# Kernel tuning notes

Measured on AMD Instinct MI355X. Metric: run time of the kernel, lower is better.

The kernel has to match this reference:

```python
import jax, jax.numpy as jnp
import numpy as np

V = 200000   # total vertices
K = 96       # neighbours per vertex (incl. self)
NSEG = 4     # number of row-split segments


def setup_inputs() -> dict:
    key = jax.random.key(0)
    k1, k2 = jax.random.split(key)
    seg_size = V // NSEG
    row_splits = (jnp.arange(NSEG + 1, dtype=jnp.int32) * seg_size)
    seg_id = jnp.repeat(jnp.arange(NSEG, dtype=jnp.int32), seg_size)
    seg_start = row_splits[seg_id]                      # (V,)
    # segment-local random neighbours, self index in column 0 (kNN convention)
    offs = jax.random.randint(k1, (V, K), 0, seg_size, dtype=jnp.int32)
    neighs = seg_start[:, None] + offs
    neighs = neighs.at[:, 0].set(jnp.arange(V, dtype=jnp.int32))
    hier = jax.random.uniform(k2, (V, 1), dtype=jnp.float32)
    return {"neighs": neighs, "hier": hier, "row_splits": row_splits}


def _cluster(neighs, hier, row_splits):
    """Greedy hierarchy-ordered neighbour clustering (NMS-like).

    Returns:
      sel     (V,1) int32: cluster-centre vertex indices, compacted to the
              front in processing order, padded with -1 (original op returns
              a dynamically sized tensor; we pad for fixed shapes).
      rs      (n_seg+1,) int32: row splits after selection.
      ggather (V,1) int32: for each vertex, the position in `sel` of its
              cluster centre (gather-back indices).
    """
    Vn, _ = neighs.shape
    n_seg = row_splits.shape[0] - 1
    seg_id = jnp.searchsorted(row_splits[1:], jnp.arange(Vn), side='right').astype(jnp.int32)
    # per-segment argsort descending on hier, with global offsets == global
    # lexsort by (segment, -hier) since vertices are segment-contiguous
    order = jnp.lexsort((-hier[:, 0], seg_id)).astype(jnp.int32)  # (V,)

    def step(assign, v):
        is_new = assign[v] < 0                 # v not yet absorbed -> new centre
        nb = neighs[v]                          # (K,) neighbour indices
        grab = is_new & (assign[nb] < 0)        # unassigned neighbours get taken
        assign = assign.at[jnp.where(is_new, v, Vn)].set(v, mode='drop')
        assign = assign.at[jnp.where(grab, nb, Vn)].set(v, mode='drop')
        return assign, is_new

    assign0 = jnp.full((Vn,), -1, jnp.int32)
    assign, is_new = jax.lax.scan(step, assign0, order)  # assign: centre vertex per vertex

    new_i = is_new.astype(jnp.int32)
    pos = jnp.cumsum(new_i) - 1                           # rank of each centre in order
    sel = jnp.full((Vn,), -1, jnp.int32).at[jnp.where(is_new, pos, Vn)].set(order, mode='drop')
    counts = jax.ops.segment_sum(new_i, seg_id[order], num_segments=n_seg)
    rs = jnp.concatenate([jnp.zeros((1,), jnp.int32), jnp.cumsum(counts).astype(jnp.int32)])
    center_rank = jnp.zeros((Vn,), jnp.int32).at[jnp.where(is_new, order, Vn)].set(pos, mode='drop')
    ggather = center_rank[assign].reshape(-1, 1)
    return sel.reshape(-1, 1), rs, ggather


def reference(neighs, hier, row_splits):
    return _cluster(neighs, hier, row_splits)
```

## Files before the change

### kernel.cpp

```cpp
#include <hip/hip_runtime.h>

#define IDX_BITS 20
#define IDX_MASK ((1u << IDX_BITS) - 1)
#define NT1 1024
#define MAX_G1 512
#define T1 49152
#define TB2 16
#define T2 4096
#define T3CAP 4096
#define GRID_ROUND_CAP 16
#define MAX_ROUNDS 8000
#define SC_CAP 1024
#define SV_CAP 4096

typedef unsigned long long u64;

__device__ __forceinline__ u64 pack_key(float h, int v) {
  return ((u64)(~__float_as_uint(h)) << IDX_BITS) | (unsigned)v;
}

__device__ __forceinline__ int ald(const int* p) {
  return __hip_atomic_load((int*)p, __ATOMIC_RELAXED, __HIP_MEMORY_SCOPE_AGENT);
}
__device__ __forceinline__ u64 ald64(const u64* p) {
  return __hip_atomic_load((u64*)p, __ATOMIC_RELAXED, __HIP_MEMORY_SCOPE_AGENT);
}
__device__ __forceinline__ void ast(int* p, int v) {
  __hip_atomic_store(p, v, __ATOMIC_RELAXED, __HIP_MEMORY_SCOPE_AGENT);
}

struct Ctx {
  const int* __restrict__ neighs;
  const float* __restrict__ hier;
  const int* __restrict__ row_splits;
  int V, K, nseg;
  u64* assign;
  int* tag;
  int* listA;
  int* listB;
  u64* centre_key;
  int* centre_v;
  int* rank_of;
  int* cnt;
  int* out_sel;
  int* out_rs;
  int* out_gg;
};

struct BlkState {
  int sc_cnt, sv_cnt, sc_base, sv_base;
  int seg_hist[8];
  int sc_list[SC_CAP];
  int sv_list[SV_CAP];
};

__device__ __forceinline__ void xbar(int* bar, int target) {
  __syncthreads();
  if (threadIdx.x == 0) {
    __builtin_amdgcn_fence(__ATOMIC_RELEASE, "agent");
    __hip_atomic_fetch_add(bar, 1, __ATOMIC_RELAXED, __HIP_MEMORY_SCOPE_AGENT);
    while (__hip_atomic_load(bar, __ATOMIC_RELAXED, __HIP_MEMORY_SCOPE_AGENT) < target)
      __builtin_amdgcn_s_sleep(2);
  }
  __syncthreads();
}

__device__ __forceinline__ void record_direct(const Ctx& c, int v, u64 pv) {
  int slot = atomicAdd(&c.cnt[4], 1);
  int seg = 0;
  for (int t = 1; t < c.nseg; ++t) seg += (v >= c.row_splits[t]);
  c.centre_v[slot] = v;
  c.centre_key[slot] = ((u64)seg << 52) | pv;
  atomicAdd(&c.cnt[8 + seg], 1);
}

__device__ __forceinline__ void phaseB(const Ctx& c, const int* rl, int an, int r,
                                       int qs, int qst, int ql) {
  if (c.K == 96) {
    for (int i = qs; i < an; i += qst) {
      int u = rl ? ald(&rl[i]) : i;
      u64 pu = pack_key(c.hier[u], u);
      if (rl && ald64(&c.assign[u]) <= pu) continue;
      const int* row = c.neighs + (size_t)u * 96;
      int w[6];
#pragma unroll
      for (int t = 0; t < 6; ++t) w[t] = row[ql + 16 * t];
#pragma unroll
      for (int t = 0; t < 6; ++t)
        if (pack_key(c.hier[w[t]], w[t]) > pu) c.tag[w[t]] = r;
    }
  } else {
    for (int i = qs; i < an; i += qst) {
      int u = rl ? ald(&rl[i]) : i;
      u64 pu = pack_key(c.hier[u], u);
      if (rl && ald64(&c.assign[u]) <= pu) continue;
      const int* row = c.neighs + (size_t)u * c.K;
      for (int j = ql; j < c.K; j += 16) {
        int w = row[j];
        if (pack_key(c.hier[w], w) > pu) c.tag[w] = r;
      }
    }
  }
}

__device__ __forceinline__ void phaseC(const Ctx& c, BlkState& bs, const int* rl,
                                       int* wl, int* survc, int an, int r,
                                       int qs, int qst, int ql) {
  for (int i = qs; i < an; i += qst) {
    int u = rl ? ald(&rl[i]) : i;
    u64 pu = pack_key(c.hier[u], u);
    if (ald64(&c.assign[u]) <= pu) continue;
    if (ald(&c.tag[u]) != r) {
      const int* row = c.neighs + (size_t)u * c.K;
      if (c.K == 96) {
#pragma unroll
        for (int t = 0; t < 6; ++t) atomicMin(&c.assign[row[ql + 16 * t]], pu);
      } else {
        for (int j = ql; j < c.K; j += 16) atomicMin(&c.assign[row[j]], pu);
      }
      if (ql == 0) {
        int s = atomicAdd(&bs.sc_cnt, 1);
        if (s < SC_CAP) bs.sc_list[s] = u; else record_direct(c, u, pu);
      }
    } else if (ql == 0) {
      u64 y = ald64(&c.assign[u]);
      if (y > pu) {
        int s = atomicAdd(&bs.sv_cnt, 1);
        if (s < SV_CAP) bs.sv_list[s] = u;
        else { int g = atomicAdd(survc, 1); wl[g] = u; }
      }
    }
  }
}

__device__ __forceinline__ void flush_block(const Ctx& c, BlkState& bs, int* wl, int* survc) {
  __syncthreads();
  int nsc = min(bs.sc_cnt, SC_CAP), nsv = min(bs.sv_cnt, SV_CAP);
  if (threadIdx.x == 0 && nsc) bs.sc_base = atomicAdd(&c.cnt[4], nsc);
  if (threadIdx.x == 0 && nsv) bs.sv_base = atomicAdd(survc, nsv);
  if (threadIdx.x < 8) bs.seg_hist[threadIdx.x] = 0;
  __syncthreads();
  for (int i = threadIdx.x; i < nsv; i += blockDim.x) wl[bs.sv_base + i] = bs.sv_list[i];
  for (int i = threadIdx.x; i < nsc; i += blockDim.x) {
    int v = bs.sc_list[i];
    int seg = 0;
    for (int t = 1; t < c.nseg; ++t) seg += (v >= c.row_splits[t]);
    c.centre_v[bs.sc_base + i] = v;
    c.centre_key[bs.sc_base + i] = ((u64)seg << 52) | pack_key(c.hier[v], v);
    atomicAdd(&bs.seg_hist[seg], 1);
  }
  __syncthreads();
  if (threadIdx.x < c.nseg) {
    int h = bs.seg_hist[threadIdx.x];
    if (h) atomicAdd(&c.cnt[8 + threadIdx.x], h);
  }
  __syncthreads();
  if (threadIdx.x == 0) { bs.sc_cnt = 0; bs.sv_cnt = 0; }
}

__global__ void __launch_bounds__(NT1) k_tier1(Ctx c) {
  __shared__ BlkState bs;
  const int tid = blockIdx.x * blockDim.x + threadIdx.x;
  const int nthr = gridDim.x * blockDim.x;
  const int ql = threadIdx.x & 15;
  const int qg = tid >> 4, nq = nthr >> 4;
  const int nb = gridDim.x;
  if (threadIdx.x == 0) { bs.sc_cnt = 0; bs.sv_cnt = 0; }
  __syncthreads();

  int aliveN = c.V, r = 0, ep = 0;
  while (true) {
    const int* rl = (r & 1) ? c.listA : c.listB;
    int* wl = (r & 1) ? c.listB : c.listA;
    if (tid == 0) ast(&c.cnt[(r + 1) & 1], 0);
    phaseB(c, r ? rl : nullptr, aliveN, r, qg, nq, ql);
    xbar(&c.cnt[16], nb * (++ep));
    phaseC(c, bs, r ? rl : nullptr, wl, &c.cnt[(r + 1) & 1], aliveN, r, qg, nq, ql);
    flush_block(c, bs, wl, &c.cnt[(r + 1) & 1]);
    xbar(&c.cnt[16], nb * (++ep));
    aliveN = ald(&c.cnt[(r + 1) & 1]);
    ++r;
    if (aliveN == 0 || aliveN <= T1 || r >= GRID_ROUND_CAP) break;
  }
  if (tid == 0) { ast(&c.cnt[5], aliveN); ast(&c.cnt[6], r); }
}

__global__ void __launch_bounds__(NT1) k_tier2(Ctx c) {
  __shared__ BlkState bs;
  const int ql = threadIdx.x & 15;
  const int NBQ = NT1 >> 4;
  if (threadIdx.x == 0) { bs.sc_cnt = 0; bs.sv_cnt = 0; }
  __syncthreads();

  int an = ald(&c.cnt[5]), tr = ald(&c.cnt[6]);
  if (an <= T2) return;

  const int qstart = blockIdx.x * NBQ + (threadIdx.x >> 4);
  const int qstride = TB2 * NBQ;
  int ep = 0;
  while (true) {
    const int* rl = (tr & 1) ? c.listA : c.listB;
    int* wl = (tr & 1) ? c.listB : c.listA;
    if (blockIdx.x == 0 && threadIdx.x == 0) ast(&c.cnt[(tr + 1) & 1], 0);
    phaseB(c, rl, an, tr, qstart, qstride, ql);
    xbar(&c.cnt[32], TB2 * (++ep));
    phaseC(c, bs, rl, wl, &c.cnt[(tr + 1) & 1], an, tr, qstart, qstride, ql);
    flush_block(c, bs, wl, &c.cnt[(tr + 1) & 1]);
    xbar(&c.cnt[32], TB2 * (++ep));
    an = ald(&c.cnt[(tr + 1) & 1]);
    ++tr;
    if (an == 0 || an <= T2 || tr >= MAX_ROUNDS) break;
  }
  if (blockIdx.x == 0 && threadIdx.x == 0) { ast(&c.cnt[5], an); ast(&c.cnt[6], tr); }
}

__global__ void __launch_bounds__(NT1) k_tier3(Ctx c) {
  __shared__ int fr[T3CAP];
  __shared__ int tg[T3CAP];
  __shared__ unsigned char dd[T3CAP];
  __shared__ int tmp[T3CAP];
  __shared__ int nnew;
  const int ql = threadIdx.x & 15;
  const int bq = threadIdx.x >> 4;
  const int NBQ = NT1 >> 4;

  int an = ald(&c.cnt[5]);
  int tr = ald(&c.cnt[6]);
  if (an <= 0 || an > T3CAP) return;
  const int* rl = (tr & 1) ? c.listA : c.listB;

  for (int i = threadIdx.x; i < an; i += NT1) {
    int v = ald(&rl[i]);
    u64 pv = pack_key(c.hier[v], v);
    fr[i] = v;
    tg[i] = -1;
    dd[i] = (ald64(&c.assign[v]) <= pv) ? 1 : 0;
    c.rank_of[v] = i;
  }
  __syncthreads();

  int r = tr;
  while (an > 0 && r < MAX_ROUNDS) {
    for (int i = bq; i < an; i += NBQ) {
      if (dd[i]) continue;
      int u = fr[i];
      u64 pu = pack_key(c.hier[u], u);
      const int* row = c.neighs + (size_t)u * c.K;
      for (int j = ql; j < c.K; j += 16) {
        int w = row[j];
        if (pack_key(c.hier[w], w) > pu) {
          int s = c.rank_of[w];
          if ((unsigned)s < (unsigned)an && fr[s] == w) tg[s] = r;
        }
      }
    }
    __syncthreads();
    for (int i = bq; i < an; i += NBQ) {
      if (dd[i]) continue;
      if (tg[i] != r) {
        int u = fr[i];
        u64 pu = pack_key(c.hier[u], u);
        const int* row = c.neighs + (size_t)u * c.K;
        for (int j = ql; j < c.K; j += 16) {
          int w = row[j];
          atomicMin(&c.assign[w], pu);
          if (pack_key(c.hier[w], w) > pu) {
            int s = c.rank_of[w];
            if ((unsigned)s < (unsigned)an && fr[s] == w) dd[s] = 1;
          }
        }
        if (ql == 0) { dd[i] = 1; record_direct(c, u, pu); }
      }
    }
    __syncthreads();
    if (threadIdx.x == 0) nnew = 0;
    __syncthreads();
    for (int i = threadIdx.x; i < an; i += NT1) {
      if (!dd[i]) { int j = atomicAdd(&nnew, 1); tmp[j] = fr[i]; }
    }
    __syncthreads();
    an = nnew;
    __syncthreads();
    for (int i = threadIdx.x; i < an; i += NT1) {
      int v = tmp[i];
      fr[i] = v; tg[i] = -1; dd[i] = 0;
      c.rank_of[v] = i;
    }
    __syncthreads();
    ++r;
  }
}

__global__ void __launch_bounds__(NT1) k_rank(Ctx c) {
  __shared__ u64 shp[NT1];
  const int nC = c.cnt[4];
  for (int base = blockIdx.x * NT1; base < nC; base += gridDim.x * NT1) {
    int idx = base + threadIdx.x;
    bool have = idx < nC;
    u64 mykey = have ? c.centre_key[idx] : 0;
    int myv = have ? c.centre_v[idx] : 0;
    int myrank = 0;
    for (int cs = 0; cs < nC; cs += NT1) {
      int j = cs + threadIdx.x;
      shp[threadIdx.x] = (j < nC) ? c.centre_key[j] : ~0ull;
      __syncthreads();
      int lim = min(NT1, nC - cs);
      for (int t = 0; t < lim; ++t) myrank += (shp[t] < mykey) ? 1 : 0;
      __syncthreads();
    }
    if (have) {
      c.out_sel[myrank] = myv;
      c.rank_of[myv] = myrank;
    }
  }
  if (blockIdx.x == 0 && threadIdx.x == 0) {
    int run = 0;
    c.out_rs[0] = 0;
    for (int s = 0; s < c.nseg; ++s) { run += c.cnt[8 + s]; c.out_rs[s + 1] = run; }
  }
}

__global__ void __launch_bounds__(256) k_gg(Ctx c) {
  int v = blockIdx.x * blockDim.x + threadIdx.x;
  const int stride = gridDim.x * blockDim.x;
  for (; v < c.V; v += stride) {
    u64 y = c.assign[v];
    u64 pv = pack_key(c.hier[v], v);
    int ctr = (y < pv) ? (int)(y & IDX_MASK) : v;
    c.out_gg[v] = c.rank_of[ctr];
  }
}

extern "C" void kernel_launch(void* const* d_in, const int* in_sizes, int n_in,
                              void* d_out, int out_size, void* d_ws, size_t ws_size,
                              hipStream_t stream) {
  Ctx c;
  c.neighs = (const int*)d_in[0];
  c.hier = (const float*)d_in[1];
  c.row_splits = (const int*)d_in[2];
  c.V = in_sizes[1];
  c.K = in_sizes[0] / c.V;
  c.nseg = in_sizes[2] - 1;

  char* pm = (char*)d_ws;
  const size_t V = (size_t)c.V;
  c.assign = (u64*)pm;        pm += V * 8;
  c.tag = (int*)pm;           pm += V * 4;
  size_t ff_bytes = V * 12;
  c.listA = (int*)pm;         pm += V * 4;
  c.listB = (int*)pm;         pm += V * 4;
  c.centre_key = (u64*)pm;    pm += V * 8;
  c.centre_v = (int*)pm;      pm += V * 4;
  c.rank_of = (int*)pm;       pm += V * 4;
  c.cnt = (int*)pm;           pm += 64 * 4;

  int* out = (int*)d_out;
  c.out_sel = out;
  c.out_rs = out + c.V;
  c.out_gg = out + c.V + c.nseg + 1;

  hipMemsetAsync(d_ws, 0xFF, ff_bytes, stream);
  hipMemsetAsync((void*)c.cnt, 0, 64 * 4, stream);
  hipMemsetAsync((void*)c.out_sel, 0xFF, V * 4, stream);

  int dev = 0, nCU = 0, maxB = 0;
  hipGetDevice(&dev);
  hipDeviceGetAttribute(&nCU, hipDeviceAttributeMultiprocessorCount, dev);
  hipOccupancyMaxActiveBlocksPerMultiprocessor(&maxB, k_tier1, NT1, 0);
  if (nCU <= 0) nCU = 256;
  if (maxB <= 0) maxB = 1;
  int g1 = nCU * maxB;
  if (g1 > MAX_G1) g1 = MAX_G1;

  void* args[] = { &c };
  hipLaunchCooperativeKernel((void*)k_tier1, dim3(g1), dim3(NT1), args, 0, stream);
  k_tier2<<<TB2, NT1, 0, stream>>>(c);
  k_tier3<<<1, NT1, 0, stream>>>(c);
  k_rank<<<16, NT1, 0, stream>>>(c);
  k_gg<<<512, 256, 0, stream>>>(c);
}
```

Baseline: 1.792 ms.

## Precompute shared-memory conflict graph for tier-3 rounds and use dead bitmask

The tier-3 single-block loop now builds, once, a compact edge list in LDS of higher-priority frontier neighbours per vertex. Each round then tags and kills vertices by walking this list instead of re-reading neighbour rows and hier values from global memory. Frontier compaction is replaced by a dead bitmask and an alive counter, and assign atomicMins for new centres are batched into a cooperative pass. The release fence in the grid barrier is dropped and plain stores become relaxed atomic stores, which risks weaker memory ordering. Edge-list overflow falls back to the old global-memory path.

```diff
diff --git a/kernel.cpp b/kernel.cpp
--- a/kernel.cpp
+++ b/kernel.cpp
@@ -8,6 +8,8 @@
 #define TB2 16
 #define T2 4096
 #define T3CAP 4096
+#define E_CAP 14336
+#define CL_CAP 1024
 #define GRID_ROUND_CAP 16
 #define MAX_ROUNDS 8000
 #define SC_CAP 1024
@@ -57,7 +59,6 @@
 __device__ __forceinline__ void xbar(int* bar, int target) {
   __syncthreads();
   if (threadIdx.x == 0) {
-    __builtin_amdgcn_fence(__ATOMIC_RELEASE, "agent");
     __hip_atomic_fetch_add(bar, 1, __ATOMIC_RELAXED, __HIP_MEMORY_SCOPE_AGENT);
     while (__hip_atomic_load(bar, __ATOMIC_RELAXED, __HIP_MEMORY_SCOPE_AGENT) < target)
       __builtin_amdgcn_s_sleep(2);
@@ -87,7 +88,7 @@
       for (int t = 0; t < 6; ++t) w[t] = row[ql + 16 * t];
 #pragma unroll
       for (int t = 0; t < 6; ++t)
-        if (pack_key(c.hier[w[t]], w[t]) > pu) c.tag[w[t]] = r;
+        if (pack_key(c.hier[w[t]], w[t]) > pu) ast(&c.tag[w[t]], r);
     }
   } else {
     for (int i = qs; i < an; i += qst) {
@@ -97,7 +98,7 @@
       const int* row = c.neighs + (size_t)u * c.K;
       for (int j = ql; j < c.K; j += 16) {
         int w = row[j];
-        if (pack_key(c.hier[w], w) > pu) c.tag[w] = r;
+        if (pack_key(c.hier[w], w) > pu) ast(&c.tag[w], r);
       }
     }
   }
@@ -127,7 +128,7 @@
       if (y > pu) {
         int s = atomicAdd(&bs.sv_cnt, 1);
         if (s < SV_CAP) bs.sv_list[s] = u;
-        else { int g = atomicAdd(survc, 1); wl[g] = u; }
+        else { int g = atomicAdd(survc, 1); ast(&wl[g], u); }
       }
     }
   }
@@ -140,7 +141,7 @@
   if (threadIdx.x == 0 && nsv) bs.sv_base = atomicAdd(survc, nsv);
   if (threadIdx.x < 8) bs.seg_hist[threadIdx.x] = 0;
   __syncthreads();
-  for (int i = threadIdx.x; i < nsv; i += blockDim.x) wl[bs.sv_base + i] = bs.sv_list[i];
+  for (int i = threadIdx.x; i < nsv; i += blockDim.x) ast(&wl[bs.sv_base + i], bs.sv_list[i]);
   for (int i = threadIdx.x; i < nsc; i += blockDim.x) {
     int v = bs.sc_list[i];
     int seg = 0;
@@ -216,33 +217,96 @@
 
 __global__ void __launch_bounds__(NT1) k_tier3(Ctx c) {
   __shared__ int fr[T3CAP];
-  __shared__ int tg[T3CAP];
-  __shared__ unsigned char dd[T3CAP];
-  __shared__ int tmp[T3CAP];
-  __shared__ int nnew;
+  __shared__ unsigned short est[T3CAP];
+  __shared__ unsigned char edeg[T3CAP];
+  __shared__ unsigned short edges[E_CAP];
+  __shared__ unsigned char tg[T3CAP];
+  __shared__ int ddb[T3CAP / 32];
+  __shared__ unsigned short cl[CL_CAP];
+  __shared__ int ecnt, aliveCnt, deaths, ncent;
+
+  const int lane = threadIdx.x & 63;
   const int ql = threadIdx.x & 15;
-  const int bq = threadIdx.x >> 4;
-  const int NBQ = NT1 >> 4;
+  const int g16 = lane >> 4;
+  const int qw = threadIdx.x >> 4;
 
   int an = ald(&c.cnt[5]);
   int tr = ald(&c.cnt[6]);
   if (an <= 0 || an > T3CAP) return;
   const int* rl = (tr & 1) ? c.listA : c.listB;
 
+  if (threadIdx.x == 0) { ecnt = 0; aliveCnt = 0; deaths = 0; ncent = 0; }
+  for (int i = threadIdx.x; i < T3CAP / 32; i += NT1) ddb[i] = 0;
+  __syncthreads();
+
   for (int i = threadIdx.x; i < an; i += NT1) {
     int v = ald(&rl[i]);
+    fr[i] = v;
+    tg[i] = 0;
     u64 pv = pack_key(c.hier[v], v);
-    fr[i] = v;
-    tg[i] = -1;
-    dd[i] = (ald64(&c.assign[v]) <= pv) ? 1 : 0;
+    if (ald64(&c.assign[v]) <= pv) atomicOr(&ddb[i >> 5], 1 << (i & 31));
+    else atomicAdd(&aliveCnt, 1);
     c.rank_of[v] = i;
   }
   __syncthreads();
 
-  int r = tr;
-  while (an > 0 && r < MAX_ROUNDS) {
-    for (int i = bq; i < an; i += NBQ) {
-      if (dd[i]) continue;
+  if (c.K == 96) {
+    for (int i = qw; i < an; i += 64) {
+      int u = fr[i];
+      u64 pu = pack_key(c.hier[u], u);
+      const int* row = c.neighs + (size_t)u * 96;
+      int sl[6]; unsigned field[6];
+#pragma unroll
+      for (int t = 0; t < 6; ++t) {
+        int w = row[ql + 16 * t];
+        int s = -1;
+        if (pack_key(c.hier[w], w) > pu) {
+          int cand = c.rank_of[w];
+          if ((unsigned)cand < (unsigned)an && fr[cand] == w) s = cand;
+        }
+        sl[t] = s;
+        u64 b = __ballot(s >= 0);
+        field[t] = (unsigned)((b >> (g16 * 16)) & 0xFFFFull);
+      }
+      int m = 0;
+#pragma unroll
+      for (int t = 0; t < 6; ++t) m += __popc(field[t]);
+      int base = 0;
+      if (ql == 0 && m) base = atomicAdd(&ecnt, m);
+      base = __shfl(base, g16 * 16, 64);
+      if (m && base + m > E_CAP) {
+        if (ql == 0) { est[i] = 0; edeg[i] = 255; }
+      } else {
+        if (ql == 0) { est[i] = (unsigned short)base; edeg[i] = (unsigned char)m; }
+        int pre = 0;
+#pragma unroll
+        for (int t = 0; t < 6; ++t) {
+          if (sl[t] >= 0) {
+            int within = __popc(field[t] & ((1u << ql) - 1));
+            edges[base + pre + within] = (unsigned short)sl[t];
+          }
+          pre += __popc(field[t]);
+        }
+      }
+    }
+  } else {
+    for (int i = threadIdx.x; i < an; i += NT1) { est[i] = 0; edeg[i] = 255; }
+  }
+  __syncthreads();
+
+  int r = 0;
+  while (aliveCnt > 0 && r < MAX_ROUNDS) {
+    unsigned char sr = (unsigned char)((r % 253) + 1);
+    for (int i = threadIdx.x; i < an; i += NT1) {
+      if ((ddb[i >> 5] >> (i & 31)) & 1) continue;
+      int d = edeg[i];
+      if (d == 255) continue;
+      int b0 = est[i];
+      for (int e = 0; e < d; ++e) tg[edges[b0 + e]] = sr;
+    }
+    for (int i = qw; i < an; i += 64) {
+      if (edeg[i] != 255) continue;
+      if ((ddb[i >> 5] >> (i & 31)) & 1) continue;
       int u = fr[i];
       u64 pu = pack_key(c.hier[u], u);
       const int* row = c.neighs + (size_t)u * c.K;
@@ -250,41 +314,61 @@
         int w = row[j];
         if (pack_key(c.hier[w], w) > pu) {
           int s = c.rank_of[w];
-          if ((unsigned)s < (unsigned)an && fr[s] == w) tg[s] = r;
+          if ((unsigned)s < (unsigned)an && fr[s] == w) tg[s] = sr;
         }
       }
     }
     __syncthreads();
-    for (int i = bq; i < an; i += NBQ) {
-      if (dd[i]) continue;
-      if (tg[i] != r) {
+    {
+      int ldeaths = 0;
+      for (int i = threadIdx.x; i < an; i += NT1) {
+        if ((ddb[i >> 5] >> (i & 31)) & 1) continue;
+        if (tg[i] == sr) continue;
         int u = fr[i];
         u64 pu = pack_key(c.hier[u], u);
-        const int* row = c.neighs + (size_t)u * c.K;
-        for (int j = ql; j < c.K; j += 16) {
-          int w = row[j];
-          atomicMin(&c.assign[w], pu);
-          if (pack_key(c.hier[w], w) > pu) {
-            int s = c.rank_of[w];
-            if ((unsigned)s < (unsigned)an && fr[s] == w) dd[s] = 1;
+        atomicOr(&ddb[i >> 5], 1 << (i & 31));
+        ++ldeaths;
+        int d = edeg[i];
+        if (d == 255) {
+          const int* row = c.neighs + (size_t)u * c.K;
+          for (int j = 0; j < c.K; ++j) {
+            int w = row[j];
+            if (pack_key(c.hier[w], w) > pu) {
+              int s = c.rank_of[w];
+              if ((unsigned)s < (unsigned)an && fr[s] == w) {
+                int old = atomicOr(&ddb[s >> 5], 1 << (s & 31));
+                if (!((old >> (s & 31)) & 1)) ++ldeaths;
+              }
+            }
+          }
+        } else {
+          int b0 = est[i];
+          for (int e = 0; e < d; ++e) {
+            int s = edges[b0 + e];
+            int old = atomicOr(&ddb[s >> 5], 1 << (s & 31));
+            if (!((old >> (s & 31)) & 1)) ++ldeaths;
           }
         }
-        if (ql == 0) { dd[i] = 1; record_direct(c, u, pu); }
-      }
+        int ci = atomicAdd(&ncent, 1);
+        if (ci < CL_CAP) cl[ci] = (unsigned short)i;
+        else {
+          const int* row = c.neighs + (size_t)u * c.K;
+          for (int j = 0; j < c.K; ++j) atomicMin(&c.assign[row[j]], pu);
+        }
+        record_direct(c, u, pu);
+      }
+      if (ldeaths) atomicAdd(&deaths, ldeaths);
     }
     __syncthreads();
-    if (threadIdx.x == 0) nnew = 0;
-    __syncthreads();
-    for (int i = threadIdx.x; i < an; i += NT1) {
-      if (!dd[i]) { int j = atomicAdd(&nnew, 1); tmp[j] = fr[i]; }
-    }
-    __syncthreads();
-    an = nnew;
-    __syncthreads();
-    for (int i = threadIdx.x; i < an; i += NT1) {
-      int v = tmp[i];
-      fr[i] = v; tg[i] = -1; dd[i] = 0;
-      c.rank_of[v] = i;
+    {
+      int nc = min(ncent, CL_CAP);
+      for (int h = qw; h < nc; h += 64) {
+        int u = fr[cl[h]];
+        u64 pu = pack_key(c.hier[u], u);
+        const int* row = c.neighs + (size_t)u * c.K;
+        for (int j = ql; j < c.K; j += 16) atomicMin(&c.assign[row[j]], pu);
+      }
+      if (threadIdx.x == 0) { aliveCnt -= deaths; deaths = 0; ncent = 0; }
     }
     __syncthreads();
     ++r;
```

Measured after the change: 1.854 ms. 3.4% more time.
